# Optimization experiments

Measured on AMD Instinct MI355X. Metric: run time of the kernel, lower is better.

Reference implementation:

```python
import jax, jax.numpy as jnp
import numpy as np

TS = (32, 32, 32)          # tensor_size per dim
NC = 32 * 32 * 32          # total grid cells
HEADS = 4


def setup_inputs() -> dict:
    key = jax.random.key(0)
    k1, k2, k3 = jax.random.split(key, 3)
    B, H, V, N = 4, HEADS, 8, 16384
    local_coordinate = jax.random.uniform(k1, (B, H, V, N), dtype=jnp.float32)
    flattened_index = jax.random.randint(k2, (B, H, V, N), 0, NC, dtype=jnp.int64)
    features = jax.random.normal(k3, (B, 128, N), dtype=jnp.float32)
    return {"local_coordinate": local_coordinate,
            "flattened_index": flattened_index,
            "features": features}


def reference(local_coordinate, flattened_index, features):
    # local_coordinate: [B, H, V, N], flattened_index: [B, H, V, N] int64
    # features: [B, H*fd, N]
    B, H, V, N = local_coordinate.shape
    fd = features.shape[1] // H
    feats = features.reshape(B, H, fd, N)
    # outer-product splat: [B, H, fd, V, N]
    pre_splat = feats[:, :, :, None, :] * local_coordinate[:, :, None, :, :]
    src = pre_splat.reshape(B, H, fd, V * N)
    idx = flattened_index.reshape(B, H, V * N)

    def scat(s, i):
        # s: [fd, V*N], i: [V*N]; out initialized to zeros like torch scatter_max with zero out
        return jnp.zeros((fd, NC), dtype=s.dtype).at[:, i].max(s)

    z = jax.vmap(jax.vmap(scat))(src, idx)  # [B, H, fd, NC]
    return z.reshape(B, H * fd, *TS)
```

## Files before the change

kernel.cpp:

```cpp
#include <hip/hip_runtime.h>
#include <hip/hip_bf16.h>

constexpr int B  = 4;
constexpr int H  = 4;
constexpr int V  = 8;
constexpr int N  = 16384;
constexpr int FD = 32;
constexpr int NC = 32768;
constexpr int BH = B * H;
constexpr int VN = V * N;
constexpr int NPAIR = BH * VN;

constexpr int CB   = 1024;
constexpr int TP   = 8192;
constexpr int SB   = NPAIR / TP;
constexpr int SUB  = SB / BH;
constexpr int CAPS = 32;
constexpr int TB   = BH * (N / 128);

typedef int   iv4 __attribute__((ext_vector_type(4)));
typedef float fv4 __attribute__((ext_vector_type(4)));

constexpr size_t OFF_CNTTAB = 0;
constexpr size_t OFF_SLOTS  = OFF_CNTTAB + (size_t)SB * CB;
constexpr size_t OFF_FEATST = OFF_SLOTS  + (size_t)SB * CB * CAPS;

__device__ __forceinline__ unsigned short f2bf(float v) {
    unsigned int u = __float_as_uint(v);
    return (unsigned short)((u + 0x7FFFu + ((u >> 16) & 1u)) >> 16);
}

__global__ __launch_bounds__(1024)
void k_prep(const int* __restrict__ idx, const float* __restrict__ lc,
            const float* __restrict__ feats, int* __restrict__ cntTab,
            unsigned int* __restrict__ slots, unsigned short* __restrict__ featsT) {
    __shared__ __align__(16) unsigned char smem[16896];
    const int tid = threadIdx.x;

    if (blockIdx.x < SB) {
        int* cursor = (int*)smem;
        cursor[tid] = 0;
        __syncthreads();

        const int blk = blockIdx.x;
        const size_t t0 = (size_t)blk * TP;
        unsigned int* myslots = slots + (size_t)blk * (CB * CAPS);

        const iv4* idx4 = (const iv4*)(idx + t0);
        const fv4* lc4  = (const fv4*)(lc + t0);
        const unsigned int nb = (unsigned int)(t0 & (N - 1));
#pragma unroll
        for (int r = 0; r < 2; ++r) {
            int i = tid + r * 1024;
            iv4 c4 = __builtin_nontemporal_load(&idx4[i]);
            fv4 l4 = __builtin_nontemporal_load(&lc4[i]);
            unsigned int n0 = nb + (unsigned int)(i * 4);
#pragma unroll
            for (int e = 0; e < 4; ++e) {
                unsigned int q = (unsigned int)(l4[e] * 8192.0f);
                unsigned int key = ((unsigned int)(c4[e] & 31) << 27)
                                 | (q << 14) | (n0 + e);
                int cb  = c4[e] >> 5;
                int pos = atomicAdd(&cursor[cb], 1);
                if (pos < CAPS)
                    myslots[cb * CAPS + pos] = key;
            }
        }
        __syncthreads();
        cntTab[blk * CB + tid] = min(cursor[tid], CAPS);
    } else {
        float (*tile)[32][33] = (float (*)[32][33])smem;
        int bi  = blockIdx.x - SB;
        int bh  = bi >> 7;
        int n0  = (bi & 127) * 128;
        int sub = tid >> 8;
        int tx  = tid & 31;
        int ty  = (tid >> 5) & 7;
        int nbase = n0 + sub * 32;
#pragma unroll
        for (int fr = 0; fr < 4; ++fr) {
            int f = ty + fr * 8;
            tile[sub][f][tx] = __builtin_nontemporal_load(
                &feats[((size_t)bh * FD + f) * N + nbase + tx]);
        }
        __syncthreads();
#pragma unroll
        for (int nr = 0; nr < 4; ++nr) {
            int n = ty + nr * 8;
            featsT[((size_t)bh * N + nbase + n) * FD + tx] = f2bf(tile[sub][tx][n]);
        }
    }
}

__global__ __launch_bounds__(256)
void k_compute(const int* __restrict__ cntTab, const unsigned int* __restrict__ slots,
               const unsigned short* __restrict__ featsT, float* __restrict__ out) {
    __shared__ unsigned int acc[32][33];
    __shared__ unsigned int kbuf[SUB * CAPS];
    __shared__ int scnt[SUB];
    __shared__ int spref[SUB + 1];
    const int tid = threadIdx.x;
    const int bh  = blockIdx.x >> 10;
    const int cb  = blockIdx.x & (CB - 1);

    if (tid < SUB)
        scnt[tid] = cntTab[(size_t)(bh * SUB + tid) * CB + cb];
    for (int i = tid; i < 32 * 33; i += 256) ((unsigned int*)acc)[i] = 0u;
    __syncthreads();
    if (tid == 0) {
        int run = 0;
#pragma unroll
        for (int s = 0; s < SUB; ++s) { spref[s] = run; run += scnt[s]; }
        spref[SUB] = run;
    }
    __syncthreads();
#pragma unroll
    for (int r = 0; r < 2; ++r) {
        int sub = (tid >> 5) + r * 8;
        int j   = tid & 31;
        if (j < scnt[sub])
            kbuf[spref[sub] + j] =
                slots[((size_t)(bh * SUB + sub) * CB + cb) * CAPS + j];
    }
    __syncthreads();

    const int cnt  = spref[SUB];
    const int last = cnt - 1;
    const int g = tid >> 5;
    const int f = tid & 31;
    const unsigned short* fT = featsT + (size_t)bh * N * FD;

    for (int r0 = 8 * g; r0 < cnt; r0 += 64) {
        unsigned int k[8];
        float fv[8];
#pragma unroll
        for (int j = 0; j < 8; ++j)
            k[j] = kbuf[min(r0 + j, last)];
#pragma unroll
        for (int j = 0; j < 8; ++j) {
            int off = (int)((k[j] & 16383u) << 5) | f;
            fv[j] = __uint_as_float((unsigned int)fT[off] << 16);
        }
#pragma unroll
        for (int j = 0; j < 8; ++j) {
            float coord = ((float)((k[j] >> 14) & 8191u) + 0.5f) * (1.0f / 8192.0f);
            float val = fmaxf(coord * fv[j], 0.0f);
            atomicMax(&acc[k[j] >> 27][f], __float_as_uint(val));
        }
    }
    __syncthreads();

    int cell = tid & 31;
    int c0   = cb * 32;
#pragma unroll
    for (int i = 0; i < 4; ++i) {
        int ff = (tid >> 5) + i * 8;
        __builtin_nontemporal_store(__uint_as_float(acc[cell][ff]),
            &out[((size_t)(bh * FD + ff)) * NC + c0 + cell]);
    }
}

extern "C" void kernel_launch(void* const* d_in, const int* in_sizes, int n_in,
                              void* d_out, int out_size, void* d_ws, size_t ws_size,
                              hipStream_t stream) {
    const float* lc    = (const float*)d_in[0];
    const int*   idx   = (const int*)  d_in[1];
    const float* feats = (const float*)d_in[2];
    float* out = (float*)d_out;

    int*            cntTab = (int*)d_ws + OFF_CNTTAB;
    unsigned int*   slots  = (unsigned int*)d_ws + OFF_SLOTS;
    unsigned short* featsT = (unsigned short*)((unsigned int*)d_ws + OFF_FEATST);

    k_prep<<<SB + TB, 1024, 0, stream>>>(idx, lc, feats, cntTab, slots, featsT);
    k_compute<<<BH * CB, 256, 0, stream>>>(cntTab, slots, featsT, out);
}
```

Before: 152.9 us.

## Shrink per-bucket slot capacity, stage slots in LDS, add overflow pass

Per-block bucket capacity drops from 32 to 14. Slots are now built in shared memory and written out with coalesced 64-bit nontemporal stores instead of scattered global writes. Entries past capacity go to a global overflow list, which a new k_overflow kernel applies afterwards with global atomicMax; this fixes the silent drop the old cap could cause. The feature transpose now uses vectorized loads and packed bf16 pair stores, and k_compute interleaves bh across block indices. The larger LDS footprint lowers prep occupancy, and overflow handling adds a memset and an extra launch.

```diff
diff --git a/kernel.cpp b/kernel.cpp
--- a/kernel.cpp
+++ b/kernel.cpp
@@ -15,37 +15,41 @@
 constexpr int TP   = 8192;
 constexpr int SB   = NPAIR / TP;
 constexpr int SUB  = SB / BH;
-constexpr int CAPS = 32;
+constexpr int CAPS = 14;
 constexpr int TB   = BH * (N / 128);
+constexpr int OFLCAP = 32768;
 
 typedef int   iv4 __attribute__((ext_vector_type(4)));
 typedef float fv4 __attribute__((ext_vector_type(4)));
 
-constexpr size_t OFF_CNTTAB = 0;
+constexpr size_t OFF_OFLCNT = 0;
+constexpr size_t OFF_OFL    = 16;
+constexpr size_t OFF_CNTTAB = OFF_OFL + 2 * (size_t)OFLCAP;
 constexpr size_t OFF_SLOTS  = OFF_CNTTAB + (size_t)SB * CB;
-constexpr size_t OFF_FEATST = OFF_SLOTS  + (size_t)SB * CB * CAPS;
-
-__device__ __forceinline__ unsigned short f2bf(float v) {
+constexpr size_t OFF_FEATST = OFF_SLOTS + (size_t)SB * CB * CAPS;
+
+__device__ __forceinline__ unsigned int f2bf(float v) {
     unsigned int u = __float_as_uint(v);
-    return (unsigned short)((u + 0x7FFFu + ((u >> 16) & 1u)) >> 16);
+    return (u + 0x7FFFu + ((u >> 16) & 1u)) >> 16;
 }
 
 __global__ __launch_bounds__(1024)
 void k_prep(const int* __restrict__ idx, const float* __restrict__ lc,
             const float* __restrict__ feats, int* __restrict__ cntTab,
-            unsigned int* __restrict__ slots, unsigned short* __restrict__ featsT) {
-    __shared__ __align__(16) unsigned char smem[16896];
+            unsigned int* __restrict__ slots, unsigned int* __restrict__ featsT32,
+            int* __restrict__ oflCnt, unsigned int* __restrict__ ofl) {
+    __shared__ __align__(16) unsigned char smem[61440];
     const int tid = threadIdx.x;
 
     if (blockIdx.x < SB) {
-        int* cursor = (int*)smem;
+        unsigned int* buf    = (unsigned int*)smem;
+        int*          cursor = (int*)(smem + CB * CAPS * 4);
         cursor[tid] = 0;
         __syncthreads();
 
         const int blk = blockIdx.x;
         const size_t t0 = (size_t)blk * TP;
-        unsigned int* myslots = slots + (size_t)blk * (CB * CAPS);
-
+        const int bh = blk >> 4;
         const iv4* idx4 = (const iv4*)(idx + t0);
         const fv4* lc4  = (const fv4*)(lc + t0);
         const unsigned int nb = (unsigned int)(t0 & (N - 1));
@@ -62,32 +66,43 @@
                                  | (q << 14) | (n0 + e);
                 int cb  = c4[e] >> 5;
                 int pos = atomicAdd(&cursor[cb], 1);
-                if (pos < CAPS)
-                    myslots[cb * CAPS + pos] = key;
+                if (pos < CAPS) {
+                    buf[cb * CAPS + pos] = key;
+                } else {
+                    int op = atomicAdd(oflCnt, 1);
+                    if (op < OFLCAP) {
+                        ofl[2 * op]     = ((unsigned int)bh << 15) | (unsigned int)c4[e];
+                        ofl[2 * op + 1] = key;
+                    }
+                }
             }
         }
         __syncthreads();
+        const unsigned long long* b64 = (const unsigned long long*)buf;
+        unsigned long long* dst =
+            (unsigned long long*)(slots + (size_t)blk * (CB * CAPS));
+#pragma unroll
+        for (int r = 0; r < CB * CAPS / 2 / 1024; ++r)
+            __builtin_nontemporal_store(b64[tid + r * 1024], &dst[tid + r * 1024]);
         cntTab[blk * CB + tid] = min(cursor[tid], CAPS);
     } else {
-        float (*tile)[32][33] = (float (*)[32][33])smem;
-        int bi  = blockIdx.x - SB;
-        int bh  = bi >> 7;
-        int n0  = (bi & 127) * 128;
-        int sub = tid >> 8;
-        int tx  = tid & 31;
-        int ty  = (tid >> 5) & 7;
-        int nbase = n0 + sub * 32;
-#pragma unroll
-        for (int fr = 0; fr < 4; ++fr) {
-            int f = ty + fr * 8;
-            tile[sub][f][tx] = __builtin_nontemporal_load(
-                &feats[((size_t)bh * FD + f) * N + nbase + tx]);
-        }
+        float (*tile)[132] = (float (*)[132])smem;
+        int bi = blockIdx.x - SB;
+        int bh = bi >> 7;
+        int n0 = (bi & 127) * 128;
+        int f  = tid >> 5, l = tid & 31;
+        fv4 v = __builtin_nontemporal_load(
+            (const fv4*)(feats + ((size_t)bh * FD + f) * N + n0 + 4 * l));
+        *(fv4*)&tile[f][4 * l] = v;
         __syncthreads();
 #pragma unroll
-        for (int nr = 0; nr < 4; ++nr) {
-            int n = ty + nr * 8;
-            featsT[((size_t)bh * N + nbase + n) * FD + tx] = f2bf(tile[sub][tx][n]);
+        for (int r = 0; r < 2; ++r) {
+            int e = tid + r * 1024;
+            int u = e & 15, n = e >> 4;
+            unsigned int lo = f2bf(tile[2 * u][n]);
+            unsigned int hi = f2bf(tile[2 * u + 1][n]);
+            __builtin_nontemporal_store(lo | (hi << 16),
+                &featsT32[((size_t)bh * N + n0 + n) * (FD / 2) + u]);
         }
     }
 }
@@ -100,11 +115,11 @@
     __shared__ int scnt[SUB];
     __shared__ int spref[SUB + 1];
     const int tid = threadIdx.x;
-    const int bh  = blockIdx.x >> 10;
-    const int cb  = blockIdx.x & (CB - 1);
+    const int bh  = blockIdx.x & 15;
+    const int cb  = blockIdx.x >> 4;
 
     if (tid < SUB)
-        scnt[tid] = cntTab[(size_t)(bh * SUB + tid) * CB + cb];
+        scnt[tid] = cntTab[(bh * SUB + tid) * CB + cb];
     for (int i = tid; i < 32 * 33; i += 256) ((unsigned int*)acc)[i] = 0u;
     __syncthreads();
     if (tid == 0) {
@@ -114,10 +129,8 @@
         spref[SUB] = run;
     }
     __syncthreads();
-#pragma unroll
-    for (int r = 0; r < 2; ++r) {
-        int sub = (tid >> 5) + r * 8;
-        int j   = tid & 31;
+    {
+        int sub = tid >> 4, j = tid & 15;
         if (j < scnt[sub])
             kbuf[spref[sub] + j] =
                 slots[((size_t)(bh * SUB + sub) * CB + cb) * CAPS + j];
@@ -157,6 +170,26 @@
         int ff = (tid >> 5) + i * 8;
         __builtin_nontemporal_store(__uint_as_float(acc[cell][ff]),
             &out[((size_t)(bh * FD + ff)) * NC + c0 + cell]);
+    }
+}
+
+__global__ __launch_bounds__(256)
+void k_overflow(const int* __restrict__ oflCnt, const unsigned int* __restrict__ ofl,
+                const unsigned short* __restrict__ featsT, unsigned int* __restrict__ out) {
+    int n_ofl = min(*oflCnt, OFLCAP);
+    int g = blockIdx.x * 8 + (threadIdx.x >> 5);
+    int f = threadIdx.x & 31;
+    for (int i = g; i < n_ofl; i += 256 * 8) {
+        unsigned int w0 = ofl[2 * i], w1 = ofl[2 * i + 1];
+        int bh = w0 >> 15, cell = (int)(w0 & 32767u);
+        int n  = (int)(w1 & 16383u);
+        float coord = ((float)((w1 >> 14) & 8191u) + 0.5f) * (1.0f / 8192.0f);
+        float fv = __uint_as_float(
+            (unsigned int)featsT[((size_t)bh * N + n) * FD + f] << 16);
+        float val = coord * fv;
+        if (val > 0.0f)
+            atomicMax(&out[((size_t)(bh * FD + f)) * NC + cell],
+                      __float_as_uint(val));
     }
 }
 
@@ -168,10 +201,16 @@
     const float* feats = (const float*)d_in[2];
     float* out = (float*)d_out;
 
+    int*            oflCnt = (int*)d_ws + OFF_OFLCNT;
+    unsigned int*   ofl    = (unsigned int*)d_ws + OFF_OFL;
     int*            cntTab = (int*)d_ws + OFF_CNTTAB;
     unsigned int*   slots  = (unsigned int*)d_ws + OFF_SLOTS;
-    unsigned short* featsT = (unsigned short*)((unsigned int*)d_ws + OFF_FEATST);
-
-    k_prep<<<SB + TB, 1024, 0, stream>>>(idx, lc, feats, cntTab, slots, featsT);
-    k_compute<<<BH * CB, 256, 0, stream>>>(cntTab, slots, featsT, out);
-}
+    unsigned int*   fT32   = (unsigned int*)d_ws + OFF_FEATST;
+    unsigned short* fT16   = (unsigned short*)fT32;
+
+    hipMemsetAsync(oflCnt, 0, sizeof(int), stream);
+    k_prep<<<SB + TB, 1024, 0, stream>>>(idx, lc, feats, cntTab, slots, fT32,
+                                         oflCnt, ofl);
+    k_compute<<<BH * CB, 256, 0, stream>>>(cntTab, slots, fT16, out);
+    k_overflow<<<256, 256, 0, stream>>>(oflCnt, ofl, fT16, (unsigned int*)out);
+}
```

Result: slower. 210.1 us (+37.4%).
